# Performance work log

Measured on AMD Instinct MI355X. Metric: run time of the kernel, lower is better.

## Reference

```python
import jax, jax.numpy as jnp
import numpy as np

K = 20  # neighbors, per get_u_xt default


def setup_inputs() -> dict:
    key = jax.random.key(0)
    ks = jax.random.split(key, 6)
    B, N, D, H = 2048, 100000, 64, 256
    return {
        "t": jax.random.uniform(ks[0], (1,), dtype=jnp.float32),
        "z": jax.random.normal(ks[1], (B, D + 2), dtype=jnp.float32),
        "data": jax.random.normal(ks[2], (N, D), dtype=jnp.float32),
        "velocity": jax.random.normal(ks[3], (N, D), dtype=jnp.float32),
        "W1": jax.random.normal(ks[4], (D + 1, H), dtype=jnp.float32) * 0.05,
        "b1": jnp.zeros((H,), dtype=jnp.float32),
        "W2": jax.random.normal(ks[5], (H, D), dtype=jnp.float32) * 0.05,
        "b2": jnp.zeros((D,), dtype=jnp.float32),
    }


def _get_u_xt(xt, x, v, k=K):
    # Euclidean cdist via ||a||^2 + ||b||^2 - 2 a.b  -> [B, N]
    sq = (jnp.sum(xt * xt, axis=1)[:, None]
          + jnp.sum(x * x, axis=1)[None, :]
          - 2.0 * (xt @ x.T))
    dists = jnp.sqrt(jnp.maximum(sq, 1e-30))
    neg_d, knn_idx = jax.lax.top_k(-dists, k)  # k smallest distances
    knn_dists = -neg_d                          # ascending order, [B, k]
    h = jnp.maximum(knn_dists[:, -1:], 1e-12)   # bandwidth = k-th NN dist
    w = jnp.exp(-knn_dists ** 2 / (2.0 * h ** 2))
    w = w / (jnp.sum(w, axis=1, keepdims=True) + 1e-12)
    v_knn = v[knn_idx]                          # gather [B, k, D]
    return jnp.einsum('bk,bkd->bd', w, v_knn)


def reference(t, z, data, velocity, W1, b1, W2, b2):
    x = z[:, :-2]                               # [B, D]
    B = x.shape[0]
    inp = jnp.concatenate([x, jnp.broadcast_to(t, (B,))[:, None]], axis=1)
    x_dot = jax.nn.relu(inp @ W1 + b1) @ W2 + b2  # MLP model(...) -> [B, D]
    u_t = _get_u_xt(x, data, velocity)
    eps = 1e-8  # torch F.cosine_similarity eps
    nu = jnp.maximum(jnp.linalg.norm(u_t, axis=1), eps)
    nx = jnp.maximum(jnp.linalg.norm(x_dot, axis=1), eps)
    cos_sim = 1.0 - jnp.sum(u_t * x_dot, axis=1) / (nu * nx)
    L2_squared = jnp.sum((u_t - x_dot) ** 2, axis=1)
    return jnp.concatenate([x_dot, cos_sim[:, None], L2_squared[:, None]], axis=1)
```

## Files before the change

kernel.cpp:

```cpp
#include <hip/hip_runtime.h>
#include <math.h>

#define B      2048
#define N      100000
#define NPAD2  100352
#define JGRP2  98
#define JGRP2P 104
#define JT4    16
#define DD     64
#define HH     256
#define KK     20
#define SAMPLE 8192
#define CAP    1024
#define SSEL   512
#define SLACK  1.5f
#define LCAP   16

#define INF_F (__builtin_inff())

typedef __bf16 bf16x8 __attribute__((ext_vector_type(8)));
typedef __bf16 bf16x4 __attribute__((ext_vector_type(4)));
typedef float  floatx4 __attribute__((ext_vector_type(4)));
union U16 { uint4 u; bf16x8 v; };

__device__ __forceinline__ float wsum64(float v) {
    #pragma unroll
    for (int o = 32; o > 0; o >>= 1) v += __shfl_xor(v, o, 64);
    return v;
}
__device__ __forceinline__ int wsum64i(int v) {
    #pragma unroll
    for (int o = 32; o > 0; o >>= 1) v += __shfl_xor(v, o, 64);
    return v;
}

#define NB_DATA 6272
#define NB_PREP 512
#define NB_MLP  256
__global__ __launch_bounds__(256) void setup_all(const float* __restrict__ z,
                                                 const float* __restrict__ tp,
                                                 const float* __restrict__ data,
                                                 const float* __restrict__ W1,
                                                 const float* __restrict__ b1,
                                                 const float* __restrict__ W2,
                                                 const float* __restrict__ b2,
                                                 float* __restrict__ xs,
                                                 float* __restrict__ xnorm,
                                                 __bf16* __restrict__ xs_h,
                                                 int* __restrict__ cnt,
                                                 float* __restrict__ dnorm,
                                                 float* __restrict__ dnh,
                                                 __bf16* __restrict__ d_hf,
                                                 float* __restrict__ xdot) {
    int bx = blockIdx.x, tid = threadIdx.x;
    if (bx < NB_DATA) {
        int gt = bx * 256 + tid;
        int j = gt >> 4, l = gt & 15;
        float4 v = make_float4(0.f, 0.f, 0.f, 0.f);
        if (j < N)
            v = reinterpret_cast<const float4*>(data + (size_t)j * 64)[l];
        bf16x4 o;
        o.x = (__bf16)v.x; o.y = (__bf16)v.y; o.z = (__bf16)v.z; o.w = (__bf16)v.w;
        size_t u4idx = (size_t)(j >> 4) * 128 + (size_t)(l >> 1) * 16 + (j & 15);
        *reinterpret_cast<bf16x4*>(reinterpret_cast<char*>(d_hf) + u4idx * 16 + (l & 1) * 8) = o;
        float s = v.x * v.x + v.y * v.y + v.z * v.z + v.w * v.w;
        #pragma unroll
        for (int o2 = 1; o2 < 16; o2 <<= 1) s += __shfl_xor(s, o2, 64);
        if (l == 0) {
            dnorm[j] = (j < N) ? s : INF_F;
            dnh[j]   = (j < N) ? 0.5f * s : INF_F;
        }
    } else if (bx < NB_DATA + NB_PREP) {
        int row = (bx - NB_DATA) * 4 + (tid >> 6);
        int d = tid & 63;
        float v = z[row * 66 + d];
        xs[row * 64 + d] = v;
        xs_h[row * 64 + d] = (__bf16)v;
        float s = wsum64(v * v);
        if (d == 0) xnorm[row] = s;
        if (d == 1) cnt[row] = 0;
    } else {
        __shared__ float sin_[8][65];
        __shared__ float shid[8][HH];
        int row0 = (bx - NB_DATA - NB_PREP) * 8;
        float tval = tp[0];
        for (int idx = tid; idx < 8 * 64; idx += 256) {
            int r = idx >> 6, d = idx & 63;
            sin_[r][d] = z[(row0 + r) * 66 + d];
        }
        if (tid < 8) sin_[tid][64] = tval;
        __syncthreads();
        int h = tid;
        float acc[8];
        #pragma unroll
        for (int r = 0; r < 8; ++r) acc[r] = b1[h];
        for (int i = 0; i < 65; ++i) {
            float wv = W1[i * HH + h];
            #pragma unroll
            for (int r = 0; r < 8; ++r) acc[r] = fmaf(sin_[r][i], wv, acc[r]);
        }
        #pragma unroll
        for (int r = 0; r < 8; ++r) shid[r][h] = fmaxf(acc[r], 0.f);
        __syncthreads();
        int d = tid & 63, rb = tid >> 6;
        for (int rr = rb; rr < 8; rr += 4) {
            float a = b2[d];
            #pragma unroll 8
            for (int hh2 = 0; hh2 < HH; ++hh2)
                a = fmaf(shid[rr][hh2], W2[hh2 * 64 + d], a);
            xdot[(size_t)(row0 + rr) * 64 + d] = a;
        }
    }
}

__global__ __launch_bounds__(256) void sample_gemm(const __bf16* __restrict__ xs_h,
                                                   const __bf16* __restrict__ d_hf,
                                                   const float* __restrict__ xnorm,
                                                   const float* __restrict__ dnorm,
                                                   unsigned short* __restrict__ samp16) {
    int tid = threadIdx.x;
    int b = blockIdx.x;
    int xcd = b & 7, i = b >> 3;
    int w = (i >> 4) * 8 + xcd;
    int r = i & 15;
    int m0 = r * 128;
    int jbase = w * 128;
    int wv = tid >> 6, wm = wv & 1, wn = wv >> 1;
    int lane = tid & 63, l16 = lane & 15, quad = lane >> 4;
    const uint4* dq = reinterpret_cast<const uint4*>(d_hf);

    bf16x8 af[2][4], bfr[2][4];
    #pragma unroll
    for (int s = 0; s < 2; ++s)
        #pragma unroll
        for (int mt = 0; mt < 4; ++mt) {
            int row = m0 + wm * 64 + mt * 16 + l16;
            U16 u; u.u = reinterpret_cast<const uint4*>(xs_h + (size_t)row * 64)[s * 4 + quad];
            af[s][mt] = u.v;
        }
    #pragma unroll
    for (int s = 0; s < 2; ++s)
        #pragma unroll
        for (int nt = 0; nt < 4; ++nt) {
            int jblk = (jbase >> 4) + wn * 4 + nt;
            U16 u; u.u = dq[(size_t)jblk * 128 + s * 64 + lane];
            bfr[s][nt] = u.v;
        }
    float dn[4], sxn[4][4];
    #pragma unroll
    for (int nt = 0; nt < 4; ++nt)
        dn[nt] = dnorm[jbase + wn * 64 + nt * 16 + l16];
    #pragma unroll
    for (int mt = 0; mt < 4; ++mt)
        #pragma unroll
        for (int rg = 0; rg < 4; ++rg)
            sxn[mt][rg] = xnorm[m0 + wm * 64 + mt * 16 + quad * 4 + rg];

    floatx4 acc[4][4];
    #pragma unroll
    for (int mt = 0; mt < 4; ++mt)
        #pragma unroll
        for (int nt = 0; nt < 4; ++nt)
            acc[mt][nt] = (floatx4){0.f, 0.f, 0.f, 0.f};
    #pragma unroll
    for (int s = 0; s < 2; ++s)
        #pragma unroll
        for (int mt = 0; mt < 4; ++mt)
            #pragma unroll
            for (int nt = 0; nt < 4; ++nt)
                acc[mt][nt] = __builtin_amdgcn_mfma_f32_16x16x32_bf16(
                    af[s][mt], bfr[s][nt], acc[mt][nt], 0, 0, 0);

    #pragma unroll
    for (int mt = 0; mt < 4; ++mt)
        #pragma unroll
        for (int nt = 0; nt < 4; ++nt) {
            floatx4 a4 = acc[mt][nt];
            int j = jbase + wn * 64 + nt * 16 + l16;
            #pragma unroll
            for (int rg = 0; rg < 4; ++rg) {
                int row = m0 + wm * 64 + mt * 16 + quad * 4 + rg;
                float sq = fmaf(a4[rg], -2.f, dn[nt]) + sxn[mt][rg];
                unsigned short key =
                    (unsigned short)(__float_as_uint(fmaxf(sq, 0.f)) >> 16);
                __builtin_nontemporal_store(key, &samp16[(size_t)row * SAMPLE + j]);
            }
        }
}

__global__ __launch_bounds__(256) void thr_select(const unsigned short* __restrict__ samp16,
                                                  float* __restrict__ thr) {
    int wv = threadIdx.x >> 6, lane = threadIdx.x & 63;
    int row = blockIdx.x * 4 + wv;
    const unsigned* sp = reinterpret_cast<const unsigned*>(samp16 + (size_t)row * SAMPLE);
    unsigned w[64];
    #pragma unroll
    for (int i = 0; i < 64; ++i) w[i] = __builtin_nontemporal_load(sp + lane + i * 64);
    unsigned res = 0;
    for (int b = 15; b >= 0; --b) {
        unsigned cand = res | (1u << b);
        int c = 0;
        #pragma unroll
        for (int i = 0; i < 64; ++i) {
            c += ((w[i] & 0xFFFFu) < cand);
            c += ((w[i] >> 16) < cand);
        }
        c = wsum64i(c);
        if (c <= KK - 1) res = cand;
    }
    if (lane == 0) thr[row] = __uint_as_float((res + 1u) << 16);
}

__global__ __launch_bounds__(256, 3) void gemm_filter(const __bf16* __restrict__ xs_h,
                                                      const __bf16* __restrict__ d_hf,
                                                      const float* __restrict__ xnorm,
                                                      const float* __restrict__ dnh,
                                                      const float* __restrict__ thr,
                                                      int* __restrict__ cnt,
                                                      float* __restrict__ bufd,
                                                      int* __restrict__ bufi) {
    __shared__ float sts[128];
    __shared__ int   lcnt[128];
    __shared__ float lbd[128][LCAP + 1];
    __shared__ int   lbj[128][LCAP + 1];
    int tid = threadIdx.x;
    int b = blockIdx.x;
    int xcd = b & 7, i = b >> 3;
    int w = (i >> 4) * 8 + xcd;
    if (w >= JGRP2) return;
    int r = i & 15;
    int m0 = r * 128;
    int jstart = w * (JT4 * 64);
    int wv = tid >> 6, wm = wv & 1, wn = wv >> 1;
    int lane = tid & 63, l16 = lane & 15, quad = lane >> 4;
    const uint4* dq = reinterpret_cast<const uint4*>(d_hf);

    if (tid < 128) {
        sts[tid] = thr[m0 + tid] + 2.0f * SLACK;
        lcnt[tid] = 0;
    }
    bf16x8 af[2][4];
    #pragma unroll
    for (int s = 0; s < 2; ++s)
        #pragma unroll
        for (int mt = 0; mt < 4; ++mt) {
            int row = m0 + wm * 64 + mt * 16 + l16;
            U16 u; u.u = reinterpret_cast<const uint4*>(xs_h + (size_t)row * 64)[s * 4 + quad];
            af[s][mt] = u.v;
        }
    float scv[4][4];
    #pragma unroll
    for (int mt = 0; mt < 4; ++mt)
        #pragma unroll
        for (int rg = 0; rg < 4; ++rg) {
            int mg = m0 + wm * 64 + mt * 16 + quad * 4 + rg;
            scv[mt][rg] = 0.5f * (thr[mg] + 2.0f * SLACK - xnorm[mg]);
        }
    __syncthreads();

    uint4 bb[2][4];
    float dh[2][2];
    {
        int jblk0 = (jstart >> 4) + wn * 2;
        #pragma unroll
        for (int s = 0; s < 2; ++s)
            #pragma unroll
            for (int nt = 0; nt < 2; ++nt)
                bb[0][s * 2 + nt] = dq[(size_t)(jblk0 + nt) * 128 + s * 64 + lane];
        #pragma unroll
        for (int nt = 0; nt < 2; ++nt)
            dh[0][nt] = dnh[jstart + wn * 32 + nt * 16 + l16];
    }

    #pragma unroll 2
    for (int t = 0; t < JT4; ++t) {
        int cur = t & 1, nxt = cur ^ 1;
        if (t + 1 < JT4) {
            int jblkb = (jstart >> 4) + (t + 1) * 4 + wn * 2;
            #pragma unroll
            for (int s = 0; s < 2; ++s)
                #pragma unroll
                for (int nt = 0; nt < 2; ++nt)
                    bb[nxt][s * 2 + nt] = dq[(size_t)(jblkb + nt) * 128 + s * 64 + lane];
            int jb = jstart + (t + 1) * 64;
            #pragma unroll
            for (int nt = 0; nt < 2; ++nt)
                dh[nxt][nt] = dnh[jb + wn * 32 + nt * 16 + l16];
        }

        floatx4 acc[4][2];
        #pragma unroll
        for (int mt = 0; mt < 4; ++mt) {
            floatx4 cv = (floatx4){scv[mt][0], scv[mt][1], scv[mt][2], scv[mt][3]};
            acc[mt][0] = cv;
            acc[mt][1] = cv;
        }
        #pragma unroll
        for (int s = 0; s < 2; ++s) {
            U16 u0, u1;
            u0.u = bb[cur][s * 2 + 0];
            u1.u = bb[cur][s * 2 + 1];
            #pragma unroll
            for (int mt = 0; mt < 4; ++mt) {
                acc[mt][0] = __builtin_amdgcn_mfma_f32_16x16x32_bf16(af[s][mt], u0.v, acc[mt][0], 0, 0, 0);
                acc[mt][1] = __builtin_amdgcn_mfma_f32_16x16x32_bf16(af[s][mt], u1.v, acc[mt][1], 0, 0, 0);
            }
        }

        int jb = jstart + t * 64;
        #pragma unroll
        for (int nt = 0; nt < 2; ++nt) {
            int j = jb + wn * 32 + nt * 16 + l16;
            float dd = dh[cur][nt];
            #pragma unroll
            for (int mt = 0; mt < 4; ++mt) {
                floatx4 a4 = acc[mt][nt];
                bool p0 = a4[0] >= dd, p1 = a4[1] >= dd;
                bool p2 = a4[2] >= dd, p3 = a4[3] >= dd;
                if (p0 | p1 | p2 | p3) {
                    #pragma unroll
                    for (int rg = 0; rg < 4; ++rg) {
                        bool pp = (rg == 0) ? p0 : (rg == 1) ? p1 : (rg == 2) ? p2 : p3;
                        if (pp) {
                            int mloc = wm * 64 + mt * 16 + quad * 4 + rg;
                            float delta = 2.0f * (dd - a4[rg]);
                            int pos = atomicAdd(&lcnt[mloc], 1);
                            if (pos < LCAP) {
                                lbd[mloc][pos] = delta;
                                lbj[mloc][pos] = j;
                            } else {
                                int row = m0 + mloc;
                                int gp = atomicAdd(&cnt[row], 1);
                                if (gp < CAP) {
                                    bufd[(size_t)row * CAP + gp] = sts[mloc] + delta;
                                    bufi[(size_t)row * CAP + gp] = j;
                                }
                            }
                        }
                    }
                }
            }
        }
    }
    __syncthreads();
    if (tid < 128) {
        int c = lcnt[tid];
        if (c > LCAP) c = LCAP;
        if (c > 0) {
            int row = m0 + tid;
            float ts = sts[tid];
            int base = atomicAdd(&cnt[row], c);
            for (int i = 0; i < c; ++i) {
                int gp = base + i;
                if (gp < CAP) {
                    bufd[(size_t)row * CAP + gp] = ts + lbd[tid][i];
                    bufi[(size_t)row * CAP + gp] = lbj[tid][i];
                }
            }
        }
    }
}

__global__ __launch_bounds__(64) void select_finish(const float* __restrict__ bufd,
                                                    const int* __restrict__ bufi,
                                                    const int* __restrict__ cnt,
                                                    const float* __restrict__ xs,
                                                    const float* __restrict__ xnorm,
                                                    const float* __restrict__ dnorm,
                                                    const float* __restrict__ data,
                                                    const float* __restrict__ xdot,
                                                    const float* __restrict__ vel,
                                                    float* __restrict__ out) {
    __shared__ float sd[CAP];
    __shared__ int   si[CAP];
    __shared__ float sx[64];
    __shared__ float se[SSEL];
    __shared__ int   sj[SSEL];
    __shared__ int   scnt;
    __shared__ float seld[KK];
    __shared__ int   seli[KK];
    __shared__ float selw[KK];
    int row = blockIdx.x, lane = threadIdx.x;
    int n = cnt[row];
    if (n > CAP) n = CAP;
    for (int i = lane; i < n; i += 64) {
        sd[i] = bufd[(size_t)row * CAP + i];
        si[i] = bufi[(size_t)row * CAP + i];
    }
    sx[lane] = xs[row * 64 + lane];
    if (lane == 0) scnt = 0;
    __syncthreads();

    unsigned res = 0;
    for (int b = 30; b >= 0; --b) {
        unsigned cand = res | (1u << b);
        int c = 0;
        for (int i = lane; i < n; i += 64)
            c += (__float_as_uint(fmaxf(sd[i], 0.f)) < cand);
        c = wsum64i(c);
        if (c <= KK - 1) res = cand;
    }
    float T = __uint_as_float(res);

    for (int i = lane; i < n; i += 64) {
        if (sd[i] <= T + 2.0f * SLACK) {
            int q = atomicAdd(&scnt, 1);
            if (q < SSEL) sj[q] = si[i];
        }
    }
    __syncthreads();
    int m = scnt < SSEL ? scnt : SSEL;
    for (int c = lane; c < m; c += 64) {
        int j = sj[c];
        const float4* dp = reinterpret_cast<const float4*>(data + (size_t)j * 64);
        float dot = 0.f;
        #pragma unroll
        for (int kb = 0; kb < 16; ++kb) {
            float4 q = dp[kb];
            dot = fmaf(sx[kb * 4 + 0], q.x, dot);
            dot = fmaf(sx[kb * 4 + 1], q.y, dot);
            dot = fmaf(sx[kb * 4 + 2], q.z, dot);
            dot = fmaf(sx[kb * 4 + 3], q.w, dot);
        }
        se[c] = xnorm[row] + dnorm[j] - 2.0f * dot;
    }
    __syncthreads();
    for (int k = 0; k < KK; ++k) {
        float v = INF_F; int id = 0x7fffffff; int p = -1;
        for (int i = lane; i < m; i += 64) {
            float x = se[i]; int xi = sj[i];
            if (x < v || (x == v && xi < id)) { v = x; id = xi; p = i; }
        }
        #pragma unroll
        for (int o = 32; o > 0; o >>= 1) {
            float ov = __shfl_xor(v, o, 64);
            int oid = __shfl_xor(id, o, 64);
            int op  = __shfl_xor(p, o, 64);
            if (ov < v || (ov == v && oid < id)) { v = ov; id = oid; p = op; }
        }
        if (lane == 0) {
            seld[k] = v; seli[k] = id;
            if (p >= 0) se[p] = INF_F;
        }
        __syncthreads();
    }
    float d20 = sqrtf(fmaxf(seld[KK - 1], 1e-30f));
    float h = fmaxf(d20, 1e-12f);
    float wk = 0.f;
    if (lane < KK) {
        float dd = sqrtf(fmaxf(seld[lane], 1e-30f));
        wk = expf(-(dd * dd) / (2.f * h * h));
    }
    float tot = wsum64(wk) + 1e-12f;
    if (lane < KK) selw[lane] = wk / tot;
    __syncthreads();
    float u = 0.f;
    #pragma unroll
    for (int k = 0; k < KK; ++k)
        u = fmaf(selw[k], vel[(size_t)seli[k] * 64 + lane], u);
    float xd = xdot[(size_t)row * 64 + lane];
    float du  = wsum64(u * xd);
    float nu2 = wsum64(u * u);
    float nx2 = wsum64(xd * xd);
    float l2  = wsum64((u - xd) * (u - xd));
    float nu = fmaxf(sqrtf(nu2), 1e-8f);
    float nx = fmaxf(sqrtf(nx2), 1e-8f);
    out[(size_t)row * 66 + lane] = xd;
    if (lane == 0) {
        out[(size_t)row * 66 + 64] = 1.f - du / (nu * nx);
        out[(size_t)row * 66 + 65] = l2;
    }
}

extern "C" void kernel_launch(void* const* d_in, const int* in_sizes, int n_in,
                              void* d_out, int out_size, void* d_ws, size_t ws_size,
                              hipStream_t stream) {
    const float* t_   = (const float*)d_in[0];
    const float* z    = (const float*)d_in[1];
    const float* data = (const float*)d_in[2];
    const float* vel  = (const float*)d_in[3];
    const float* W1   = (const float*)d_in[4];
    const float* b1   = (const float*)d_in[5];
    const float* W2   = (const float*)d_in[6];
    const float* b2   = (const float*)d_in[7];
    float* out = (float*)d_out;

    float*  xs    = (float*)d_ws;
    float*  xnorm = xs + 131072;
    float*  thr   = xnorm + 2048;
    int*    cnt   = (int*)(thr + 2048);
    float*  xdot  = (float*)(cnt + 2048);
    float*  dnorm = xdot + 131072;
    float*  dnh   = dnorm + NPAD2;
    __bf16* xs_h  = (__bf16*)(dnh + NPAD2);
    __bf16* d_hf  = xs_h + 131072;
    unsigned short* samp16 = (unsigned short*)(d_hf + (size_t)NPAD2 * 64);
    float*  bufd  = (float*)samp16;
    int*    bufi  = (int*)(bufd + (size_t)B * CAP);

    setup_all<<<NB_DATA + NB_PREP + NB_MLP, 256, 0, stream>>>(
        z, t_, data, W1, b1, W2, b2, xs, xnorm, xs_h, cnt, dnorm, dnh, d_hf, xdot);
    sample_gemm<<<1024, 256, 0, stream>>>(xs_h, d_hf, xnorm, dnorm, samp16);
    thr_select<<<B / 4, 256, 0, stream>>>(samp16, thr);
    gemm_filter<<<16 * JGRP2P, 256, 0, stream>>>(
        xs_h, d_hf, xnorm, dnh, thr, cnt, bufd, bufi);
    select_finish<<<B, 64, 0, stream>>>(bufd, bufi, cnt, xs, xnorm, dnorm, data,
                                        xdot, vel, out);
    (void)ws_size; (void)in_sizes; (void)n_in; (void)out_size;
}
```

Baseline: 305.1 us.

## Stage sample keys in LDS for coalesced stores; widen filter GEMM tile

sample_gemm now writes its 16-bit distance keys into a shared-memory tile first, then stores each row with 128-bit vector nontemporal writes. This replaces scattered 2-byte global stores. gemm_filter widens each wave's column tile from 32 to 64 (128 columns per iteration, 8 iterations instead of 16) and drops the occupancy hint of 3 blocks per SM. The wider tile means more MFMA work per B-operand load, but it raises register pressure and may lower occupancy.

```diff
diff --git a/kernel.cpp b/kernel.cpp
--- a/kernel.cpp
+++ b/kernel.cpp
@@ -6,7 +6,7 @@
 #define NPAD2  100352
 #define JGRP2  98
 #define JGRP2P 104
-#define JT4    16
+#define JT8    8
 #define DD     64
 #define HH     256
 #define KK     20
@@ -21,6 +21,7 @@
 typedef __bf16 bf16x8 __attribute__((ext_vector_type(8)));
 typedef __bf16 bf16x4 __attribute__((ext_vector_type(4)));
 typedef float  floatx4 __attribute__((ext_vector_type(4)));
+typedef unsigned uix4 __attribute__((ext_vector_type(4)));
 union U16 { uint4 u; bf16x8 v; };
 
 __device__ __forceinline__ float wsum64(float v) {
@@ -118,6 +119,7 @@
                                                    const float* __restrict__ xnorm,
                                                    const float* __restrict__ dnorm,
                                                    unsigned short* __restrict__ samp16) {
+    __shared__ unsigned short skey[128][136];
     int tid = threadIdx.x;
     int b = blockIdx.x;
     int xcd = b & 7, i = b >> 3;
@@ -176,16 +178,25 @@
         #pragma unroll
         for (int nt = 0; nt < 4; ++nt) {
             floatx4 a4 = acc[mt][nt];
-            int j = jbase + wn * 64 + nt * 16 + l16;
+            int jloc = wn * 64 + nt * 16 + l16;
             #pragma unroll
             for (int rg = 0; rg < 4; ++rg) {
-                int row = m0 + wm * 64 + mt * 16 + quad * 4 + rg;
+                int rowloc = wm * 64 + mt * 16 + quad * 4 + rg;
                 float sq = fmaf(a4[rg], -2.f, dn[nt]) + sxn[mt][rg];
-                unsigned short key =
+                skey[rowloc][jloc] =
                     (unsigned short)(__float_as_uint(fmaxf(sq, 0.f)) >> 16);
-                __builtin_nontemporal_store(key, &samp16[(size_t)row * SAMPLE + j]);
             }
         }
+    __syncthreads();
+    {
+        int row = tid >> 1, half = tid & 1;
+        const uix4* src = reinterpret_cast<const uix4*>(&skey[row][half * 64]);
+        unsigned short* gp = samp16 + (size_t)(m0 + row) * SAMPLE + jbase + half * 64;
+        uix4* dst = reinterpret_cast<uix4*>(gp);
+        #pragma unroll
+        for (int q = 0; q < 8; ++q)
+            __builtin_nontemporal_store(src[q], &dst[q]);
+    }
 }
 
 __global__ __launch_bounds__(256) void thr_select(const unsigned short* __restrict__ samp16,
@@ -211,14 +222,14 @@
     if (lane == 0) thr[row] = __uint_as_float((res + 1u) << 16);
 }
 
-__global__ __launch_bounds__(256, 3) void gemm_filter(const __bf16* __restrict__ xs_h,
-                                                      const __bf16* __restrict__ d_hf,
-                                                      const float* __restrict__ xnorm,
-                                                      const float* __restrict__ dnh,
-                                                      const float* __restrict__ thr,
-                                                      int* __restrict__ cnt,
-                                                      float* __restrict__ bufd,
-                                                      int* __restrict__ bufi) {
+__global__ __launch_bounds__(256) void gemm_filter(const __bf16* __restrict__ xs_h,
+                                                   const __bf16* __restrict__ d_hf,
+                                                   const float* __restrict__ xnorm,
+                                                   const float* __restrict__ dnh,
+                                                   const float* __restrict__ thr,
+                                                   int* __restrict__ cnt,
+                                                   float* __restrict__ bufd,
+                                                   int* __restrict__ bufi) {
     __shared__ float sts[128];
     __shared__ int   lcnt[128];
     __shared__ float lbd[128][LCAP + 1];
@@ -230,7 +241,7 @@
     if (w >= JGRP2) return;
     int r = i & 15;
     int m0 = r * 128;
-    int jstart = w * (JT4 * 64);
+    int jstart = w * (JT8 * 128);
     int wv = tid >> 6, wm = wv & 1, wn = wv >> 1;
     int lane = tid & 63, l16 = lane & 15, quad = lane >> 4;
     const uint4* dq = reinterpret_cast<const uint4*>(d_hf);
@@ -258,59 +269,59 @@
         }
     __syncthreads();
 
-    uint4 bb[2][4];
-    float dh[2][2];
+    uint4 bb[2][8];
+    float dh[2][4];
     {
-        int jblk0 = (jstart >> 4) + wn * 2;
+        int jblk0 = (jstart >> 4) + wn * 4;
         #pragma unroll
         for (int s = 0; s < 2; ++s)
             #pragma unroll
-            for (int nt = 0; nt < 2; ++nt)
-                bb[0][s * 2 + nt] = dq[(size_t)(jblk0 + nt) * 128 + s * 64 + lane];
-        #pragma unroll
-        for (int nt = 0; nt < 2; ++nt)
-            dh[0][nt] = dnh[jstart + wn * 32 + nt * 16 + l16];
+            for (int nt = 0; nt < 4; ++nt)
+                bb[0][s * 4 + nt] = dq[(size_t)(jblk0 + nt) * 128 + s * 64 + lane];
+        #pragma unroll
+        for (int nt = 0; nt < 4; ++nt)
+            dh[0][nt] = dnh[jstart + wn * 64 + nt * 16 + l16];
     }
 
     #pragma unroll 2
-    for (int t = 0; t < JT4; ++t) {
+    for (int t = 0; t < JT8; ++t) {
         int cur = t & 1, nxt = cur ^ 1;
-        if (t + 1 < JT4) {
-            int jblkb = (jstart >> 4) + (t + 1) * 4 + wn * 2;
+        if (t + 1 < JT8) {
+            int jblkb = (jstart >> 4) + (t + 1) * 8 + wn * 4;
             #pragma unroll
             for (int s = 0; s < 2; ++s)
                 #pragma unroll
-                for (int nt = 0; nt < 2; ++nt)
-                    bb[nxt][s * 2 + nt] = dq[(size_t)(jblkb + nt) * 128 + s * 64 + lane];
-            int jb = jstart + (t + 1) * 64;
-            #pragma unroll
-            for (int nt = 0; nt < 2; ++nt)
-                dh[nxt][nt] = dnh[jb + wn * 32 + nt * 16 + l16];
-        }
-
-        floatx4 acc[4][2];
+                for (int nt = 0; nt < 4; ++nt)
+                    bb[nxt][s * 4 + nt] = dq[(size_t)(jblkb + nt) * 128 + s * 64 + lane];
+            int jb = jstart + (t + 1) * 128;
+            #pragma unroll
+            for (int nt = 0; nt < 4; ++nt)
+                dh[nxt][nt] = dnh[jb + wn * 64 + nt * 16 + l16];
+        }
+
+        floatx4 acc[4][4];
         #pragma unroll
         for (int mt = 0; mt < 4; ++mt) {
             floatx4 cv = (floatx4){scv[mt][0], scv[mt][1], scv[mt][2], scv[mt][3]};
-            acc[mt][0] = cv;
-            acc[mt][1] = cv;
+            #pragma unroll
+            for (int nt = 0; nt < 4; ++nt)
+                acc[mt][nt] = cv;
         }
         #pragma unroll
         for (int s = 0; s < 2; ++s) {
-            U16 u0, u1;
-            u0.u = bb[cur][s * 2 + 0];
-            u1.u = bb[cur][s * 2 + 1];
-            #pragma unroll
-            for (int mt = 0; mt < 4; ++mt) {
-                acc[mt][0] = __builtin_amdgcn_mfma_f32_16x16x32_bf16(af[s][mt], u0.v, acc[mt][0], 0, 0, 0);
-                acc[mt][1] = __builtin_amdgcn_mfma_f32_16x16x32_bf16(af[s][mt], u1.v, acc[mt][1], 0, 0, 0);
+            #pragma unroll
+            for (int nt = 0; nt < 4; ++nt) {
+                U16 u0; u0.u = bb[cur][s * 4 + nt];
+                #pragma unroll
+                for (int mt = 0; mt < 4; ++mt)
+                    acc[mt][nt] = __builtin_amdgcn_mfma_f32_16x16x32_bf16(af[s][mt], u0.v, acc[mt][nt], 0, 0, 0);
             }
         }
 
-        int jb = jstart + t * 64;
-        #pragma unroll
-        for (int nt = 0; nt < 2; ++nt) {
-            int j = jb + wn * 32 + nt * 16 + l16;
+        int jb = jstart + t * 128;
+        #pragma unroll
+        for (int nt = 0; nt < 4; ++nt) {
+            int j = jb + wn * 64 + nt * 16 + l16;
             float dd = dh[cur][nt];
             #pragma unroll
             for (int mt = 0; mt < 4; ++mt) {
```

Result: slower. 444.5 us (+45.7%).
